# Kernel optimization log

Measured on AMD Instinct MI355X. Metric: run time of the kernel, lower is better.

The kernel has to match this reference:

```python
import jax, jax.numpy as jnp
import numpy as np

# ---- grid / frustum config (matches init_kwargs) ----
XB = (-50.0, 50.0, 0.5); YB = (-50.0, 50.0, 0.5); ZB = (-10.0, 10.0, 20.0); DB = (4.0, 45.0, 1.0)
OGFH, OGFW = 128, 352
DOWNSAMPLE = 16
FH, FW = OGFH // DOWNSAMPLE, OGFW // DOWNSAMPLE  # 8, 22
DD = int(round((DB[1] - DB[0]) / DB[2]))         # 41 depth bins
DX = jnp.array([XB[2], YB[2], ZB[2]], jnp.float32)
BX = jnp.array([XB[0] + XB[2] / 2.0, YB[0] + YB[2] / 2.0, ZB[0] + ZB[2] / 2.0], jnp.float32)
NX = (int(round((XB[1] - XB[0]) / XB[2])), int(round((YB[1] - YB[0]) / YB[2])), int(round((ZB[1] - ZB[0]) / ZB[2])))  # (200,200,1)
UNDISTORT_ITERS = 20


def _frustum():
    # [DD, FH, FW, 3] pixel (x, y) + candidate depth, as in create_frustum
    ds = jnp.arange(DB[0], DB[1], DB[2], dtype=jnp.float32)[:, None, None]
    xs = jnp.linspace(0.0, OGFW - 1.0, FW, dtype=jnp.float32)[None, None, :]
    ys = jnp.linspace(0.0, OGFH - 1.0, FH, dtype=jnp.float32)[None, :, None]
    shp = (DD, FH, FW)
    return jnp.stack([jnp.broadcast_to(xs, shp), jnp.broadcast_to(ys, shp), jnp.broadcast_to(ds, shp)], axis=-1)


def setup_inputs() -> dict:
    B, N, C = 8, 6, 64
    key = jax.random.key(0)
    ks = jax.random.split(key, 6)
    depth_logits = jax.random.normal(ks[0], (B, N, DD, FH, FW), jnp.float32)
    feats = jax.random.normal(ks[1], (B, N, C, FH, FW), jnp.float32)
    # camera->ego rotation: cam z(forward)->ego x, cam x(right)->-ego y, cam y(down)->-ego z
    R = jnp.array([[0.0, 0.0, 1.0], [-1.0, 0.0, 0.0], [0.0, -1.0, 0.0]], jnp.float32)
    rots = jnp.broadcast_to(R, (B, N, 3, 3))
    trans = jax.random.normal(ks[2], (B, N, 3), jnp.float32) * 0.5
    gamma = 400.0 * (1.0 + 0.05 * jax.random.uniform(ks[3], (B, N, 2), jnp.float32))
    K = jnp.concatenate([gamma, jnp.full((B, N, 1), 176.0), jnp.full((B, N, 1), 64.0)], axis=-1)
    Dcoef = jax.random.normal(ks[4], (B, N, 4), jnp.float32) * 0.01
    xi = 0.9 + 0.05 * jax.random.uniform(ks[5], (B, N), jnp.float32)
    return {"depth_logits": depth_logits, "feats": feats, "rots": rots, "trans": trans, "K": K, "Dcoef": Dcoef, "xi": xi}


def reference(depth_logits, feats, rots, trans, K, Dcoef, xi):
    B, N, Dd, H, W = depth_logits.shape
    C = feats.shape[2]
    frustum = _frustum()  # [Dd,H,W,3]
    pix_x = jnp.broadcast_to(frustum[None, None, ..., 0], (B, N, Dd, H, W))
    pix_y = jnp.broadcast_to(frustum[None, None, ..., 1], (B, N, Dd, H, W))
    depth_cand = frustum[None, None, ..., 2:3]  # [1,1,Dd,H,W,1]

    def v5(a):
        return a[:, :, None, None, None]

    g1, g2, u0, v0 = (v5(K[..., i]) for i in range(4))
    k1, k2, p1, p2 = (v5(Dcoef[..., i]) for i in range(4))
    xiv = v5(xi)
    # MEI-model iterative undistortion
    ppx = (pix_x - u0) / g1
    ppy = (pix_y - v0) / g2
    pux, puy = ppx, ppy
    for _ in range(UNDISTORT_ITERS):
        r2 = pux * pux + puy * puy
        r4 = r2 * r2
        denom = 1.0 + k1 * r2 + k2 * r4
        nx_ = (ppx - 2.0 * p1 * pux * puy - p2 * (r2 + 2.0 * pux * pux)) / denom
        ny_ = (ppy - 2.0 * p2 * pux * puy - p1 * (r2 + 2.0 * puy * puy)) / denom
        pux, puy = nx_, ny_
    r2 = pux * pux + puy * puy
    a = r2 + 1.0
    b = 2.0 * xiv * r2
    c = xiv * xiv * r2 - 1.0
    Zs = (-b + jnp.sqrt(b * b - 4.0 * a * c)) / (2.0 * a)
    rays = jnp.stack([pux * (Zs + xiv), puy * (Zs + xiv), Zs], axis=-1)
    rays = rays / jnp.sqrt(jnp.sum(rays * rays, axis=-1, keepdims=True))
    pts_cam = rays * depth_cand  # [B,N,Dd,H,W,3]
    pts_ego = jnp.einsum('bnij,bndhwj->bndhwi', rots, pts_cam) + trans[:, :, None, None, None, :]

    # fisheye circle mask [B,N,H,W]
    yy, xx = jnp.meshgrid(jnp.arange(H, dtype=jnp.float32), jnp.arange(W, dtype=jnp.float32), indexing='ij')
    u0m = jnp.floor(K[..., 2] / DOWNSAMPLE)[..., None, None]
    v0m = jnp.floor(K[..., 3] / DOWNSAMPLE)[..., None, None]
    radius = (min(H, W) - 1) // 2
    mask = ((xx - u0m) ** 2 + (yy - v0m) ** 2) >= float(radius * radius)
    maskD = mask[:, :, None, :, :]  # broadcast over depth bins

    pts_ego = jnp.where(maskD[..., None], -1000.0, pts_ego)
    pts_ego = pts_ego * jnp.array([-1.0, 1.0, 1.0], pts_ego.dtype)  # flip x

    # lift: depth distribution x context features -> [B,N,Dd,H,W,C]
    depth = jax.nn.softmax(depth_logits, axis=2)
    lifted = jnp.einsum('bndhw,bnchw->bndhwc', depth, feats)
    lifted = jnp.where(maskD[..., None], 0.0, lifted)

    # voxel pooling (scatter-sum; same math as sort+cumsum trick)
    Np = B * N * Dd * H * W
    xflat = lifted.reshape(Np, C)
    idx = jnp.floor((pts_ego - (BX - DX / 2.0)) / DX).astype(jnp.int32).reshape(Np, 3)
    bix = jnp.arange(Np, dtype=jnp.int32) // (Np // B)
    ix, iy, iz = idx[:, 0], idx[:, 1], idx[:, 2]
    kept = (ix >= 0) & (ix < NX[0]) & (iy >= 0) & (iy < NX[1]) & (iz >= 0) & (iz < NX[2])
    nseg = B * NX[2] * NX[0] * NX[1]
    seg = ((bix * NX[2] + iz) * NX[0] + ix) * NX[1] + iy
    seg = jnp.where(kept, seg, nseg)  # dump dropped points into extra segment
    pooled = jax.ops.segment_sum(xflat, seg, num_segments=nseg + 1)[:nseg]  # [B*Z*X*Y, C]
    bev = pooled.reshape(B, NX[2], NX[0], NX[1], C).transpose(0, 4, 1, 2, 3)  # [B,C,Z,X,Y]
    bev = bev.reshape(B, C * NX[2], NX[0], NX[1])  # unbind z + cat on channels
    return bev
```

## Files before the change

kernel.cpp:

```cpp
#include <hip/hip_runtime.h>

#define DD_   41
#define FH_   8
#define FW_   22
#define NPIX  176
#define C_    64
#define NXX   200
#define NXY   200
#define NCAM  48
#define NCHUNK 5
#define CHROWS 40
#define CAPCH  640
#define CPLANE (CHROWS*NXY)
#define NACT  25
#define NSTAGE (NACT*DD_)

__global__ __launch_bounds__(256) void k01_prep(
    const float* __restrict__ depth_logits,
    const float* __restrict__ rots,
    const float* __restrict__ trans,
    const float* __restrict__ Kp,
    const float* __restrict__ Dc,
    const float* __restrict__ xip,
    int* __restrict__ cnt_cam,
    uint2* __restrict__ bucketed)
{
#pragma clang fp contract(off)
    const int cam = blockIdx.x;
    const int t = threadIdx.x;

    __shared__ uint2 rec_stage[NSTAGE];
    __shared__ double rayx[NACT], rayy[NACT], rayz[NACT];
    __shared__ float mx_l[NACT], ss_l[NACT];
    __shared__ int pix_l[NACT];
    __shared__ int cur_lds[NCHUNK];

    for (int i = t; i < NSTAGE; i += 256) rec_stage[i] = make_uint2(0xFFFFFFFFu, 0u);
    if (t < NCHUNK) cur_lds[t] = 0;

    if (t < NACT) {
        const double u0 = (double)Kp[cam * 4 + 2];
        const double v0 = (double)Kp[cam * 4 + 3];
        const int u0m = (int)floor(u0 / 16.0);
        const int v0m = (int)floor(v0 / 16.0);
        const int dx = t % 5 - 2, dy = t / 5 - 2;
        const int w = u0m + dx, h = v0m + dy;
        const bool ok = (dx * dx + dy * dy < 9) & (w >= 0) & (w < FW_) & (h >= 0) & (h < FH_);
        pix_l[t] = ok ? h * FW_ + w : -1;
        if (ok) {
            const int pix = h * FW_ + w;
            const double g1 = (double)Kp[cam * 4 + 0];
            const double g2 = (double)Kp[cam * 4 + 1];
            const double k1 = (double)Dc[cam * 4 + 0];
            const double k2 = (double)Dc[cam * 4 + 1];
            const double p1 = (double)Dc[cam * 4 + 2];
            const double p2 = (double)Dc[cam * 4 + 3];
            const double xiv = (double)xip[cam];

            const double px = (double)w * (351.0 / 21.0);
            const double py = (double)h * (127.0 / 7.0);
            const double ppx = (px - u0) / g1;
            const double ppy = (py - v0) / g2;
            double pux = ppx, puy = ppy;
            for (int it = 0; it < 20; ++it) {
                double r2 = pux * pux + puy * puy;
                double r4 = r2 * r2;
                double denom = 1.0 + k1 * r2 + k2 * r4;
                double nx_ = (ppx - 2.0 * p1 * pux * puy - p2 * (r2 + 2.0 * pux * pux)) / denom;
                double ny_ = (ppy - 2.0 * p2 * pux * puy - p1 * (r2 + 2.0 * puy * puy)) / denom;
                pux = nx_; puy = ny_;
            }
            double r2 = pux * pux + puy * puy;
            double aq = r2 + 1.0;
            double bq = 2.0 * xiv * r2;
            double cq = xiv * xiv * r2 - 1.0;
            double Zs = (-bq + sqrt(bq * bq - 4.0 * aq * cq)) / (2.0 * aq);
            double rx = pux * (Zs + xiv);
            double ry = puy * (Zs + xiv);
            double rz = Zs;
            double nrm = sqrt(rx * rx + ry * ry + rz * rz);
            rayx[t] = rx / nrm; rayy[t] = ry / nrm; rayz[t] = rz / nrm;

            const float* lg = depth_logits + (size_t)cam * DD_ * NPIX + pix;
            float mxv = -3.0e38f;
            #pragma unroll
            for (int d = 0; d < DD_; ++d) mxv = fmaxf(mxv, lg[d * NPIX]);
            float ssum = 0.0f;
            #pragma unroll
            for (int d = 0; d < DD_; ++d) ssum += expf(lg[d * NPIX] - mxv);
            mx_l[t] = mxv; ss_l[t] = ssum;
        }
    }
    __syncthreads();

    {
        const int n = cam % 6;
        const float* R = rots + (size_t)cam * 9;
        const double R0 = (double)R[0], R1 = (double)R[1], R2 = (double)R[2];
        const double R3 = (double)R[3], R4 = (double)R[4], R5 = (double)R[5];
        const double R6 = (double)R[6], R7 = (double)R[7], R8 = (double)R[8];
        const double T0 = (double)trans[cam * 3 + 0];
        const double T1 = (double)trans[cam * 3 + 1];
        const double T2 = (double)trans[cam * 3 + 2];
        for (int i = t; i < NSTAGE; i += 256) {
            const int s = i / DD_, d = i - s * DD_;
            const int pix = pix_l[s];
            if (pix < 0) continue;
            const float lgv = depth_logits[((size_t)cam * DD_ + d) * NPIX + pix];
            const float wgt = expf(lgv - mx_l[s]) / ss_l[s];
            const double dval = 4.0 + (double)d;
            const double pcx = rayx[s] * dval, pcy = rayy[s] * dval, pcz = rayz[s] * dval;
            const double ex = R0 * pcx + R1 * pcy + R2 * pcz + T0;
            const double ey = R3 * pcx + R4 * pcy + R5 * pcz + T1;
            const double ez = R6 * pcx + R7 * pcy + R8 * pcz + T2;
            const double sx = -ex, sy = ey, sz = ez;
            const int ix = (int)floor((sx + 50.0) / 0.5);
            const int iy = (int)floor((sy + 50.0) / 0.5);
            const int iz = (int)floor((sz + 10.0) / 20.0);
            if ((ix >= 0) & (ix < NXX) & (iy >= 0) & (iy < NXY) & (iz == 0)) {
                unsigned meta = (unsigned)iy | ((unsigned)ix << 8)
                              | ((unsigned)pix << 16) | ((unsigned)n << 24);
                rec_stage[i] = make_uint2(meta, __float_as_uint(wgt));
            }
        }
    }
    __syncthreads();

    for (int i = t; i < NSTAGE; i += 256) {
        uint2 r = rec_stage[i];
        if (r.x != 0xFFFFFFFFu) {
            int chunk = (int)((r.x >> 8) & 255u) / CHROWS;
            int pos = atomicAdd(&cur_lds[chunk], 1);
            if (pos < CAPCH)
                bucketed[((size_t)cam * NCHUNK + chunk) * CAPCH + pos] = r;
        }
    }
    __syncthreads();
    if (t < NCHUNK) cnt_cam[cam * NCHUNK + t] = min(cur_lds[t], CAPCH);
}

__global__ __launch_bounds__(256) void k2_splat(
    const uint2* __restrict__ bucketed,
    const int* __restrict__ cnt_cam,
    const float* __restrict__ feats,
    float* __restrict__ out)
{
    const int chunk = blockIdx.x;
    const int c     = blockIdx.y;
    const int b     = blockIdx.z;
    const int tid = threadIdx.x;
    const int ix0 = chunk * CHROWS;

    int nr[6], maxnr = 0;
    #pragma unroll
    for (int n = 0; n < 6; ++n) {
        int v = cnt_cam[(b * 6 + n) * NCHUNK + chunk];
        nr[n] = v < CAPCH ? v : CAPCH;
        maxnr = nr[n] > maxnr ? nr[n] : maxnr;
    }

    float* obase = out + (size_t)(b * C_ + c) * (NXX * NXY) + (size_t)ix0 * NXY;

    if (maxnr == 0) {
        const float4 z = make_float4(0.f, 0.f, 0.f, 0.f);
        for (int i4 = tid; i4 < CPLANE / 4; i4 += 256)
            ((float4*)obase)[i4] = z;
        return;
    }

    __shared__ float tile[CPLANE];
    for (int i4 = tid; i4 < CPLANE / 4; i4 += 256)
        ((float4*)tile)[i4] = make_float4(0.f, 0.f, 0.f, 0.f);
    __syncthreads();

    for (int q = tid; q < maxnr; q += 256) {
        #pragma unroll
        for (int n = 0; n < 6; ++n) {
            if (q < nr[n]) {
                uint2 r = bucketed[((size_t)(b * 6 + n) * NCHUNK + chunk) * CAPCH + q];
                int iy = r.x & 255, ix = (r.x >> 8) & 255;
                int hw = (r.x >> 16) & 255;
                float wgt = __uint_as_float(r.y);
                float f = feats[((size_t)(b * 6 + n) * C_ + c) * NPIX + hw];
                atomicAdd(&tile[(ix - ix0) * NXY + iy], wgt * f);
            }
        }
    }
    __syncthreads();

    for (int i4 = tid; i4 < CPLANE / 4; i4 += 256)
        ((float4*)obase)[i4] = *(const float4*)&tile[i4 * 4];
}

extern "C" void kernel_launch(void* const* d_in, const int* in_sizes, int n_in,
                              void* d_out, int out_size, void* d_ws, size_t ws_size,
                              hipStream_t stream) {
    const float* depth_logits = (const float*)d_in[0];
    const float* feats        = (const float*)d_in[1];
    const float* rots         = (const float*)d_in[2];
    const float* trans        = (const float*)d_in[3];
    const float* Kp           = (const float*)d_in[4];
    const float* Dc           = (const float*)d_in[5];
    const float* xip          = (const float*)d_in[6];
    float* out = (float*)d_out;

    char* ws = (char*)d_ws;
    int*   cnt_cam  = (int*)ws;                        ws += 8192;
    uint2* bucketed = (uint2*)ws;

    k01_prep<<<dim3(NCAM), dim3(256), 0, stream>>>(depth_logits, rots, trans,
                                                   Kp, Dc, xip, cnt_cam, bucketed);
    k2_splat<<<dim3(NCHUNK, C_, 8), dim3(256), 0, stream>>>(bucketed, cnt_cam, feats, out);
}
```

Baseline: 46.64 us.

## Fuse prep and splat kernels into one cooperative persistent kernel with grid sync

Merges the geometry/bucketing kernel and the splat kernel into a single cooperative launch. The first 48 blocks do the per-camera geometry, then a grid-wide sync, then all blocks loop over the splat tiles persistently. The goal is to remove the second kernel launch and the gap between the two kernels. In exchange it adds grid.sync overhead, an occupancy query on the host each call, and fewer resident blocks than the original 2560-block splat grid. The two-kernel path is kept as a fallback.

```diff
diff --git a/kernel.cpp b/kernel.cpp
--- a/kernel.cpp
+++ b/kernel.cpp
@@ -1,4 +1,6 @@
 #include <hip/hip_runtime.h>
+#include <hip/hip_cooperative_groups.h>
+namespace cg = cooperative_groups;
 
 #define DD_   41
 #define FH_   8
@@ -14,27 +16,23 @@
 #define CPLANE (CHROWS*NXY)
 #define NACT  25
 #define NSTAGE (NACT*DD_)
-
-__global__ __launch_bounds__(256) void k01_prep(
+#define NTILES (NCHUNK*C_*8)
+
+__device__ __forceinline__ void geometry_block(
     const float* __restrict__ depth_logits,
     const float* __restrict__ rots,
     const float* __restrict__ trans,
     const float* __restrict__ Kp,
     const float* __restrict__ Dc,
     const float* __restrict__ xip,
+    int cam, int t,
+    uint2* rec_stage,
+    double* rayx, double* rayy, double* rayz,
+    float* mx_l, float* ss_l, int* pix_l, int* cur_lds,
     int* __restrict__ cnt_cam,
     uint2* __restrict__ bucketed)
 {
 #pragma clang fp contract(off)
-    const int cam = blockIdx.x;
-    const int t = threadIdx.x;
-
-    __shared__ uint2 rec_stage[NSTAGE];
-    __shared__ double rayx[NACT], rayy[NACT], rayz[NACT];
-    __shared__ float mx_l[NACT], ss_l[NACT];
-    __shared__ int pix_l[NACT];
-    __shared__ int cur_lds[NCHUNK];
-
     for (int i = t; i < NSTAGE; i += 256) rec_stage[i] = make_uint2(0xFFFFFFFFu, 0u);
     if (t < NCHUNK) cur_lds[t] = 0;
 
@@ -139,17 +137,18 @@
     if (t < NCHUNK) cnt_cam[cam * NCHUNK + t] = min(cur_lds[t], CAPCH);
 }
 
-__global__ __launch_bounds__(256) void k2_splat(
+__device__ __forceinline__ void splat_tile(
+    int wk, int t,
     const uint2* __restrict__ bucketed,
     const int* __restrict__ cnt_cam,
     const float* __restrict__ feats,
-    float* __restrict__ out)
-{
-    const int chunk = blockIdx.x;
-    const int c     = blockIdx.y;
-    const int b     = blockIdx.z;
-    const int tid = threadIdx.x;
-    const int ix0 = chunk * CHROWS;
+    float* __restrict__ out,
+    float* tile)
+{
+    const int chunk = wk % NCHUNK;
+    const int c     = (wk / NCHUNK) % C_;
+    const int b     = wk / (NCHUNK * C_);
+    const int ix0   = chunk * CHROWS;
 
     int nr[6], maxnr = 0;
     #pragma unroll
@@ -163,17 +162,17 @@
 
     if (maxnr == 0) {
         const float4 z = make_float4(0.f, 0.f, 0.f, 0.f);
-        for (int i4 = tid; i4 < CPLANE / 4; i4 += 256)
+        for (int i4 = t; i4 < CPLANE / 4; i4 += 256)
             ((float4*)obase)[i4] = z;
         return;
     }
 
-    __shared__ float tile[CPLANE];
-    for (int i4 = tid; i4 < CPLANE / 4; i4 += 256)
+    __syncthreads();
+    for (int i4 = t; i4 < CPLANE / 4; i4 += 256)
         ((float4*)tile)[i4] = make_float4(0.f, 0.f, 0.f, 0.f);
     __syncthreads();
 
-    for (int q = tid; q < maxnr; q += 256) {
+    for (int q = t; q < maxnr; q += 256) {
         #pragma unroll
         for (int n = 0; n < 6; ++n) {
             if (q < nr[n]) {
@@ -188,8 +187,75 @@
     }
     __syncthreads();
 
-    for (int i4 = tid; i4 < CPLANE / 4; i4 += 256)
+    for (int i4 = t; i4 < CPLANE / 4; i4 += 256)
         ((float4*)obase)[i4] = *(const float4*)&tile[i4 * 4];
+}
+
+__global__ __launch_bounds__(256, 4) void fused(
+    const float* __restrict__ depth_logits,
+    const float* __restrict__ feats,
+    const float* __restrict__ rots,
+    const float* __restrict__ trans,
+    const float* __restrict__ Kp,
+    const float* __restrict__ Dc,
+    const float* __restrict__ xip,
+    int* __restrict__ cnt_cam,
+    uint2* __restrict__ bucketed,
+    float* __restrict__ out)
+{
+    __shared__ float smem[CPLANE];
+    __shared__ double rayx[NACT], rayy[NACT], rayz[NACT];
+    __shared__ float mx_l[NACT], ss_l[NACT];
+    __shared__ int pix_l[NACT];
+    __shared__ int cur_lds[NCHUNK];
+
+    const int t = threadIdx.x;
+    cg::grid_group grid = cg::this_grid();
+
+    if (blockIdx.x < NCAM) {
+        geometry_block(depth_logits, rots, trans, Kp, Dc, xip,
+                       blockIdx.x, t, (uint2*)smem,
+                       rayx, rayy, rayz, mx_l, ss_l, pix_l, cur_lds,
+                       cnt_cam, bucketed);
+        __threadfence();
+    }
+
+    grid.sync();
+
+    for (int wk = blockIdx.x; wk < NTILES; wk += gridDim.x)
+        splat_tile(wk, t, bucketed, cnt_cam, feats, out, smem);
+}
+
+__global__ __launch_bounds__(256) void k01_prep(
+    const float* __restrict__ depth_logits,
+    const float* __restrict__ rots,
+    const float* __restrict__ trans,
+    const float* __restrict__ Kp,
+    const float* __restrict__ Dc,
+    const float* __restrict__ xip,
+    int* __restrict__ cnt_cam,
+    uint2* __restrict__ bucketed)
+{
+    __shared__ uint2 rec_stage[NSTAGE];
+    __shared__ double rayx[NACT], rayy[NACT], rayz[NACT];
+    __shared__ float mx_l[NACT], ss_l[NACT];
+    __shared__ int pix_l[NACT];
+    __shared__ int cur_lds[NCHUNK];
+    geometry_block(depth_logits, rots, trans, Kp, Dc, xip,
+                   blockIdx.x, threadIdx.x, rec_stage,
+                   rayx, rayy, rayz, mx_l, ss_l, pix_l, cur_lds,
+                   cnt_cam, bucketed);
+}
+
+__global__ __launch_bounds__(256) void k2_splat(
+    const uint2* __restrict__ bucketed,
+    const int* __restrict__ cnt_cam,
+    const float* __restrict__ feats,
+    float* __restrict__ out)
+{
+    __shared__ float tile[CPLANE];
+    const int wk = blockIdx.x + NCHUNK * (blockIdx.y + C_ * blockIdx.z);
+    splat_tile(wk, threadIdx.x, bucketed, cnt_cam, feats, out, tile);
 }
 
 extern "C" void kernel_launch(void* const* d_in, const int* in_sizes, int n_in,
@@ -208,7 +274,22 @@
     int*   cnt_cam  = (int*)ws;                        ws += 8192;
     uint2* bucketed = (uint2*)ws;
 
-    k01_prep<<<dim3(NCAM), dim3(256), 0, stream>>>(depth_logits, rots, trans,
-                                                   Kp, Dc, xip, cnt_cam, bucketed);
-    k2_splat<<<dim3(NCHUNK, C_, 8), dim3(256), 0, stream>>>(bucketed, cnt_cam, feats, out);
-}
+    int perCU = 0;
+    hipError_t oerr = hipOccupancyMaxActiveBlocksPerMultiprocessor(&perCU, fused, 256, 0);
+    int nwg = (oerr == hipSuccess) ? perCU * 256 : 0;
+    if (nwg > 1024) nwg = 1024;
+
+    hipError_t lerr = hipErrorUnknown;
+    if (nwg >= NCAM) {
+        void* args[] = { (void*)&depth_logits, (void*)&feats, (void*)&rots, (void*)&trans,
+                         (void*)&Kp, (void*)&Dc, (void*)&xip,
+                         (void*)&cnt_cam, (void*)&bucketed, (void*)&out };
+        lerr = hipLaunchCooperativeKernel((const void*)fused, dim3(nwg), dim3(256),
+                                          args, 0, stream);
+    }
+    if (lerr != hipSuccess) {
+        k01_prep<<<dim3(NCAM), dim3(256), 0, stream>>>(depth_logits, rots, trans,
+                                                       Kp, Dc, xip, cnt_cam, bucketed);
+        k2_splat<<<dim3(NCHUNK, C_, 8), dim3(256), 0, stream>>>(bucketed, cnt_cam, feats, out);
+    }
+}
```

Result: slower. 97.84 us (+109.8%).
